# Optimization experiments

Measured on AMD Instinct MI355X. Metric: run time of the kernel, lower is better.

The kernel has to match this reference:

```python
import jax, jax.numpy as jnp
import numpy as np

WS = 8          # window_size
NH = 8          # num_heads
VD = 512        # values_dim
CD = 128        # coords_dim
INNER = 512     # inner_ratio * values_dim
E = INNER // NH # head_dim = 64
B, Hh, Ww_ = 2, 224, 224

# relative position indices (static)
_idx = np.array([[x, y] for x in range(WS) for y in range(WS)])
_rel = _idx[None, :, :] - _idx[:, None, :] + WS - 1  # (WS^2, WS^2, 2)
REL0 = jnp.asarray(_rel[:, :, 0])
REL1 = jnp.asarray(_rel[:, :, 1])

# shifted-window masks (static)
_s = WS * (WS // 2)
_rm = np.zeros((WS * WS, WS * WS), np.float32)
_rm[-_s:, :-_s] = -np.inf
_rm[:-_s, -_s:] = -np.inf
_cm = _rm.reshape(WS, WS, WS, WS).transpose(1, 0, 3, 2).reshape(WS * WS, WS * WS)
ROW_MASK = jnp.asarray(_rm)
COL_MASK = jnp.asarray(_cm)


def _rmsnorm(x, g, eps=1e-6):
    return x * g * jax.lax.rsqrt(jnp.mean(x * x, axis=-1, keepdims=True) + eps)


def _to_windows(x, b, Wh, Ww):
    # x: (b, hp, wp, INNER) with channel layout (e H) (head fastest)
    x = x.reshape(b, Wh, WS, Ww, WS, E, NH)
    return x.transpose(0, 6, 1, 3, 2, 4, 5).reshape(b, NH, Wh, Ww, WS * WS, E)


def setup_inputs() -> dict:
    key = jax.random.key(0)
    ks = jax.random.split(key, 8)
    s = 0.02
    return {
        "embedded_values": jax.random.normal(ks[0], (B, Hh, Ww_, VD), jnp.float32),
        "embedded_coords": jax.random.normal(ks[1], (B, Hh, Ww_, CD), jnp.float32),
        "Wqk_v": jax.random.normal(ks[2], (VD, 2 * INNER), jnp.float32) * s,
        "bqk_v": jnp.zeros((2 * INNER,), jnp.float32),
        "g_v": jnp.ones((2 * INNER,), jnp.float32),
        "Wv": jax.random.normal(ks[3], (VD, INNER), jnp.float32) * s,
        "bv": jnp.zeros((INNER,), jnp.float32),
        "Wqk_c": jax.random.normal(ks[4], (CD, 2 * INNER), jnp.float32) * s,
        "bqk_c": jnp.zeros((2 * INNER,), jnp.float32),
        "g_c": jnp.ones((2 * INNER,), jnp.float32),
        "pos_emb": jax.random.normal(ks[5], (2 * WS - 1, 2 * WS - 1), jnp.float32),
        "Wout": jax.random.normal(ks[6], (INNER, VD), jnp.float32) * s,
        "bout": jnp.zeros((VD,), jnp.float32),
    }


def reference(embedded_values, embedded_coords, Wqk_v, bqk_v, g_v, Wv, bv,
              Wqk_c, bqk_c, g_c, pos_emb, Wout, bout):
    b, h, w, _ = embedded_values.shape
    # projections; torch concat then rearrange '(d k)' k=3 interleaves channels -> reshape (..., INNER, 3)
    vqk = _rmsnorm(embedded_values @ Wqk_v + bqk_v, g_v)          # (b,h,w,2*INNER)
    vval = embedded_values @ Wv + bv                               # (b,h,w,INNER)
    v = jnp.concatenate([vqk, vval], axis=-1).reshape(b, h, w, INNER, 3)
    c = _rmsnorm(embedded_coords @ Wqk_c + bqk_c, g_c).reshape(b, h, w, INNER, 2)

    pad_h = (-h) % WS
    pad_w = (-w) % WS
    v = jnp.pad(v, ((0, 0), (0, pad_h), (0, pad_w), (0, 0), (0, 0)))
    c = jnp.pad(c, ((0, 0), (0, pad_h), (0, pad_w), (0, 0), (0, 0)))
    # shifted=True: roll windows by half window (no inverse roll in original)
    v = jnp.roll(v, (-(WS // 2), -(WS // 2)), axis=(1, 2))
    c = jnp.roll(c, (-(WS // 2), -(WS // 2)), axis=(1, 2))

    hp, wp = h + pad_h, w + pad_w
    Wh, Ww = hp // WS, wp // WS
    qv = _to_windows(v[..., 0], b, Wh, Ww)
    kv = _to_windows(v[..., 1], b, Wh, Ww)
    vv = _to_windows(v[..., 2], b, Wh, Ww)
    qc = _to_windows(c[..., 0], b, Wh, Ww)
    kc = _to_windows(c[..., 1], b, Wh, Ww)

    scale = float(E) ** 0.5
    dots = (jnp.einsum('bhijpe,bhijqe->bhijpq', qv, kv)
            + jnp.einsum('bhijpe,bhijqe->bhijpq', qc, kc)) / scale
    dots = dots + pos_emb[REL0, REL1]
    # shifted-window masks on last window row / column
    dots = dots.at[:, :, -1, :].add(ROW_MASK)
    dots = dots.at[:, :, :, -1].add(COL_MASK)

    attn = jax.nn.softmax(dots, axis=-1)
    y = jnp.einsum('bhijpq,bhijqe->bhijpe', attn, vv)
    # un-window; output channel layout is (H e) (head slow)
    y = y.reshape(b, NH, Wh, Ww, WS, WS, E).transpose(0, 2, 4, 3, 5, 1, 6)
    y = y.reshape(b, hp, wp, INNER)[:, :h, :w, :]
    return y @ Wout + bout
```

## Files before the change

### kernel.cpp

```cpp
#include <hip/hip_runtime.h>


using u16 = unsigned short;
typedef short bf16x8 __attribute__((ext_vector_type(8)));
typedef float f32x4 __attribute__((ext_vector_type(4)));
typedef u16 u16x4 __attribute__((ext_vector_type(4)));
typedef u16 u16x8 __attribute__((ext_vector_type(8)));

__device__ __forceinline__ float bf2f(u16 v) {
  return __uint_as_float(((unsigned)v) << 16);
}
__device__ __forceinline__ u16 f2bf(float f) {
  unsigned u = __float_as_uint(f);
  u += 0x7fffu + ((u >> 16) & 1u);
  return (u16)(u >> 16);
}

__device__ __forceinline__ void gld16(const u16* g, u16* l) {
  __builtin_amdgcn_global_load_lds(
      (const __attribute__((address_space(1))) unsigned*)g,
      (__attribute__((address_space(3))) unsigned*)l, 16, 0, 0);
}

struct f8 { float v[8]; };
__device__ __forceinline__ f8 ld8(const float* p) {
  f8 r;
  *(float4*)&r.v[0] = *(const float4*)p;
  *(float4*)&r.v[4] = *(const float4*)(p + 4);
  return r;
}
__device__ __forceinline__ bf16x8 nfrag(u16x8 raw, const f8& A, const f8& B, float s) {
  u16x8 o;
#pragma unroll
  for (int j = 0; j < 8; ++j) o[j] = f2bf(bf2f(raw[j]) * (A.v[j] * s + B.v[j]));
  return *(bf16x8*)&o;
}
__device__ __forceinline__ bf16x8 nfragA(u16x8 raw, const f8& A, float s) {
  u16x8 o;
#pragma unroll
  for (int j = 0; j < 8; ++j) o[j] = f2bf(bf2f(raw[j]) * (A.v[j] * s));
  return *(bf16x8*)&o;
}

__global__ void conv_bf16(const float* __restrict__ in, u16* __restrict__ out) {
  size_t i = ((size_t)blockIdx.x * 256 + threadIdx.x) * 8;
  float4 a = *(const float4*)(in + i);
  float4 b = *(const float4*)(in + i + 4);
  u16x8 o;
  o[0] = f2bf(a.x); o[1] = f2bf(a.y); o[2] = f2bf(a.z); o[3] = f2bf(a.w);
  o[4] = f2bf(b.x); o[5] = f2bf(b.y); o[6] = f2bf(b.z); o[7] = f2bf(b.w);
  *(u16x8*)(out + i) = o;
}

__global__ void prep_wv(const float* __restrict__ Wqkv, const float* __restrict__ Wv,
                        u16* __restrict__ out) {
  int idx = blockIdx.x * 256 + threadIdx.x;
  if (idx >= 1536 * 512) return;
  int j = idx >> 9, kk = idx & 511;
  int t = j >> 9, rr = j & 511, nn = rr >> 6, e = rr & 63;
  int cc = 3 * (e * 8 + nn) + t;
  float v = (cc < 1024) ? Wqkv[kk * 1024 + cc] : Wv[kk * 512 + (cc - 1024)];
  out[idx] = f2bf(v);
}

__global__ void prep_wc(const float* __restrict__ W, u16* __restrict__ out) {
  int idx = blockIdx.x * 256 + threadIdx.x;
  if (idx >= 1024 * 128) return;
  int j = idx >> 7, kk = idx & 127;
  int t = j >> 9, rr = j & 511, nn = rr >> 6, e = rr & 63;
  int cc = 2 * (e * 8 + nn) + t;
  out[idx] = f2bf(W[kk * 1024 + cc]);
}

__global__ void prep_wout(const float* __restrict__ W, u16* __restrict__ out) {
  int idx = blockIdx.x * 256 + threadIdx.x;
  if (idx >= 512 * 512) return;
  int o = idx >> 9, kk = idx & 511;
  out[idx] = f2bf(W[kk * 512 + o]);
}

__global__ void prep_vec(const float* __restrict__ bqkv, const float* __restrict__ g_v,
                         const float* __restrict__ bv, const float* __restrict__ bqkc,
                         const float* __restrict__ g_c,
                         float* __restrict__ bpv, float* __restrict__ gAv, float* __restrict__ gBv,
                         float* __restrict__ bpc, float* __restrict__ gAc, float* __restrict__ gBc) {
  int j = blockIdx.x * 256 + threadIdx.x;
  if (j < 1536) {
    int t = j >> 9, rr = j & 511, nn = rr >> 6, e = rr & 63;
    int cc = 3 * (e * 8 + nn) + t;
    if (cc < 1024) { bpv[j] = bqkv[cc]; gAv[j] = g_v[cc]; gBv[j] = 0.f; }
    else           { bpv[j] = bv[cc - 1024]; gAv[j] = 0.f; gBv[j] = 1.f; }
  }
  if (j < 1024) {
    int t = j >> 9, rr = j & 511, nn = rr >> 6, e = rr & 63;
    int cc = 2 * (e * 8 + nn) + t;
    bpc[j] = bqkc[cc]; gAc[j] = g_c[cc]; gBc[j] = 0.f;
  }
}

__global__ void prep_biasT(const float* __restrict__ pe, float* __restrict__ bT) {
  int idx = blockIdx.x * 256 + threadIdx.x;
  if (idx >= 4 * 4096) return;
  int v = idx >> 12, q = (idx >> 6) & 63, p = idx & 63;
  int ap = p >> 3, bp = p & 7, aq = q >> 3, bq = q & 7;
  float val = pe[(aq - ap + 7) * 15 + (bq - bp + 7)];
  if ((v & 1) && ((ap >= 4) != (aq >= 4))) val = -1e30f;
  if ((v & 2) && ((bp >= 4) != (bq >= 4))) val = -1e30f;
  bT[idx] = val;
}

template<int N, int K, int MODE>
__global__ __launch_bounds__(256, 4) void gemm_bt(
    const u16* __restrict__ A, const u16* __restrict__ Bt,
    const float* __restrict__ bias, void* __restrict__ outp,
    float* __restrict__ part, const float* __restrict__ gB, int nwg) {
  constexpr int NCB = N / 128;
  constexpr int KT = K / 32;
  const int orig = blockIdx.x;
  const int work = (orig & 7) * (nwg >> 3) + (orig >> 3);
  const int bm = work / NCB, bn = work % NCB;

  const int tid = threadIdx.x;
  const int w = tid >> 6;
  const int lane = tid & 63;
  const int wr = w >> 1, wc = w & 1;
  const int g = lane >> 4, c = lane & 15;

  __shared__ u16 As[2 * 4096];
  __shared__ u16 Bs[2 * 4096];

  f32x4 acc[4][4] = {};
  const u16* Ag = A + (size_t)bm * 128 * K;
  const u16* Bg = Bt + (size_t)bn * 128 * K;

  auto stage = [&](int buf, int kt) {
    const int k0 = kt * 32;
#pragma unroll
    for (int i = 0; i < 2; ++i) {
      const int idx = i * 256 + tid;
      const int row = idx >> 2, ch = idx & 3;
      const int sch = ch ^ ((row >> 1) & 3);
      gld16(Ag + (size_t)row * K + k0 + sch * 8, As + buf * 4096 + idx * 8);
      gld16(Bg + (size_t)row * K + k0 + sch * 8, Bs + buf * 4096 + idx * 8);
    }
  };

  stage(0, 0);
  __syncthreads();

  const int swz = (c >> 1) & 3;
  for (int kt = 0; kt < KT; ++kt) {
    if (kt + 1 < KT) stage((kt + 1) & 1, kt + 1);
    const u16* Ab = As + (kt & 1) * 4096;
    const u16* Bb = Bs + (kt & 1) * 4096;
    bf16x8 af[4], bfv[4];
#pragma unroll
    for (int mi = 0; mi < 4; ++mi)
      af[mi] = *(const bf16x8*)(Ab + (wr * 64 + mi * 16 + c) * 32 + (g ^ swz) * 8);
#pragma unroll
    for (int ni = 0; ni < 4; ++ni)
      bfv[ni] = *(const bf16x8*)(Bb + (wc * 64 + ni * 16 + c) * 32 + (g ^ swz) * 8);
#pragma unroll
    for (int mi = 0; mi < 4; ++mi)
#pragma unroll
      for (int ni = 0; ni < 4; ++ni)
        acc[mi][ni] = __builtin_amdgcn_mfma_f32_16x16x32_bf16(bfv[ni], af[mi], acc[mi][ni], 0, 0, 0);
    __syncthreads();
  }

  const int rowbase = bm * 128 + wr * 64;
  const int colbase = bn * 128 + wc * 64;
  if constexpr (MODE == 0) {
    u16* O = (u16*)outp;
    float rowsq[4] = {0.f, 0.f, 0.f, 0.f};
#pragma unroll
    for (int ni = 0; ni < 4; ++ni) {
      const int col4 = colbase + ni * 16 + g * 4;
      const float4 bb = *(const float4*)(bias + col4);
      const float4 gb = *(const float4*)(gB + col4);
#pragma unroll
      for (int mi = 0; mi < 4; ++mi) {
        const int row = rowbase + mi * 16 + c;
        u16x4 pk;
        float v0 = acc[mi][ni][0] + bb.x;
        float v1 = acc[mi][ni][1] + bb.y;
        float v2 = acc[mi][ni][2] + bb.z;
        float v3 = acc[mi][ni][3] + bb.w;
        pk[0] = f2bf(v0); pk[1] = f2bf(v1); pk[2] = f2bf(v2); pk[3] = f2bf(v3);
        *(u16x4*)(O + (size_t)row * N + col4) = pk;
        rowsq[mi] += (gb.x == 0.f ? v0 * v0 : 0.f) + (gb.y == 0.f ? v1 * v1 : 0.f)
                   + (gb.z == 0.f ? v2 * v2 : 0.f) + (gb.w == 0.f ? v3 * v3 : 0.f);
      }
    }
#pragma unroll
    for (int mi = 0; mi < 4; ++mi) {
      float s = rowsq[mi];
      s += __shfl_xor(s, 16);
      s += __shfl_xor(s, 32);
      rowsq[mi] = s;
    }
    float* red = (float*)As;
    if (g == 0) {
#pragma unroll
      for (int mi = 0; mi < 4; ++mi)
        red[wc * 128 + wr * 64 + mi * 16 + c] = rowsq[mi];
    }
    __syncthreads();
    if (tid < 128)
      part[(size_t)(bm * 128 + tid) * NCB + bn] = red[tid] + red[128 + tid];
  } else {
    float* O = (float*)outp;
#pragma unroll
    for (int ni = 0; ni < 4; ++ni) {
      const int col4 = colbase + ni * 16 + g * 4;
      const float4 bb = *(const float4*)(bias + col4);
#pragma unroll
      for (int mi = 0; mi < 4; ++mi) {
        const int row = rowbase + mi * 16 + c;
        f32x4 o;
        o[0] = acc[mi][ni][0] + bb.x;
        o[1] = acc[mi][ni][1] + bb.y;
        o[2] = acc[mi][ni][2] + bb.z;
        o[3] = acc[mi][ni][3] + bb.w;
        *(f32x4*)(O + (size_t)row * N + col4) = o;
      }
    }
  }
}

__global__ void combine_scales(const float* __restrict__ pvp, const float* __restrict__ pcp,
                               float* __restrict__ sv, float* __restrict__ sc) {
  const int i = blockIdx.x * 256 + threadIdx.x;
  float s = 0.f;
#pragma unroll
  for (int k = 0; k < 12; ++k) s += pvp[(size_t)i * 12 + k];
  sv[i] = rsqrtf(s * (1.f / 1024.f) + 1e-6f);
  float s2 = 0.f;
#pragma unroll
  for (int k = 0; k < 8; ++k) s2 += pcp[(size_t)i * 8 + k];
  sc[i] = rsqrtf(s2 * (1.f / 1024.f) + 1e-6f);
}

__global__ __launch_bounds__(64) void attn_kernel(
    const u16* __restrict__ Pv, const u16* __restrict__ Pc,
    const float* __restrict__ sv, const float* __restrict__ sc,
    const float* __restrict__ gAv, const float* __restrict__ gBv,
    const float* __restrict__ gAc, const float* __restrict__ gBc,
    const float* __restrict__ biasT, u16* __restrict__ Y) {
  const int l = threadIdx.x;
  int bx = blockIdx.x;
  const int wj = bx % 28; bx /= 28;
  const int wi = bx % 28; bx /= 28;
  const int n = bx & 7;
  const int bi = bx >> 3;

  const int g = l >> 4, c = l & 15;
  const int rr0 = l >> 3, rch = l & 7;

  __shared__ u16 Vl[64 * 72];
  __shared__ u16 Pl[64 * 72];

  auto pixof = [&](int a, int b2) -> int {
    int y = wi * 8 + a + 4; if (y >= 224) y -= 224;
    int x = wj * 8 + b2 + 4; if (x >= 224) x -= 224;
    return (bi * 224 + y) * 224 + x;
  };

  int pixr[4]; float svr[4], scr[4];
#pragma unroll
  for (int r = 0; r < 4; ++r) {
    const int p = r * 16 + c;
    pixr[r] = pixof(p >> 3, p & 7);
    svr[r] = sv[pixr[r]];
    scr[r] = sc[pixr[r]];
  }

  u16x8 vreg[8]; float vs_[8];
#pragma unroll
  for (int i = 0; i < 8; ++i) {
    const int pix = pixof(i, rr0);
    vs_[i] = sv[pix];
    vreg[i] = *(const u16x8*)(Pv + (size_t)pix * 1536 + 1024 + n * 64 + rch * 8);
  }

  f32x4 acc[4][4] = {};
#pragma unroll
  for (int kk = 0; kk < 2; ++kk) {
    const int e0 = kk * 32 + g * 8;
    const f8 qA = ld8(gAv + n * 64 + e0), qB = ld8(gBv + n * 64 + e0);
    const f8 kA = ld8(gAv + 512 + n * 64 + e0), kB = ld8(gBv + 512 + n * 64 + e0);
    bf16x8 af[4], bq[4];
#pragma unroll
    for (int r = 0; r < 4; ++r) {
      const u16* src = Pv + (size_t)pixr[r] * 1536 + n * 64 + e0;
      af[r] = nfrag(*(const u16x8*)(src + 512), kA, kB, svr[r]);
      bq[r] = nfrag(*(const u16x8*)src, qA, qB, svr[r]);
    }
#pragma unroll
    for (int mi = 0; mi < 4; ++mi)
#pragma unroll
      for (int ni = 0; ni < 4; ++ni)
        acc[mi][ni] = __builtin_amdgcn_mfma_f32_16x16x32_bf16(af[mi], bq[ni], acc[mi][ni], 0, 0, 0);
  }
#pragma unroll
  for (int kk = 0; kk < 2; ++kk) {
    const int e0 = kk * 32 + g * 8;
    const f8 qA = ld8(gAc + n * 64 + e0);
    const f8 kA = ld8(gAc + 512 + n * 64 + e0);
    bf16x8 af[4], bq[4];
#pragma unroll
    for (int r = 0; r < 4; ++r) {
      const u16* src = Pc + (size_t)pixr[r] * 1024 + n * 64 + e0;
      af[r] = nfragA(*(const u16x8*)(src + 512), kA, scr[r]);
      bq[r] = nfragA(*(const u16x8*)src, qA, scr[r]);
    }
#pragma unroll
    for (int mi = 0; mi < 4; ++mi)
#pragma unroll
      for (int ni = 0; ni < 4; ++ni)
        acc[mi][ni] = __builtin_amdgcn_mfma_f32_16x16x32_bf16(af[mi], bq[ni], acc[mi][ni], 0, 0, 0);
  }

  const int variant = ((wi == 27) ? 1 : 0) | ((wj == 27) ? 2 : 0);
  const float* BT = biasT + variant * 4096;
#pragma unroll
  for (int mi = 0; mi < 4; ++mi)
#pragma unroll
    for (int ni = 0; ni < 4; ++ni)
#pragma unroll
      for (int r = 0; r < 4; ++r) {
        const int q = mi * 16 + g * 4 + r;
        const int p = ni * 16 + c;
        acc[mi][ni][r] = acc[mi][ni][r] * 0.125f + BT[q * 64 + p];
      }
  float rinv[4];
#pragma unroll
  for (int ni = 0; ni < 4; ++ni) {
    float m = -3.0e38f;
#pragma unroll
    for (int mi = 0; mi < 4; ++mi)
#pragma unroll
      for (int r = 0; r < 4; ++r) m = fmaxf(m, acc[mi][ni][r]);
    m = fmaxf(m, __shfl_xor(m, 16));
    m = fmaxf(m, __shfl_xor(m, 32));
    float ssum = 0.f;
#pragma unroll
    for (int mi = 0; mi < 4; ++mi)
#pragma unroll
      for (int r = 0; r < 4; ++r) {
        float e = __expf(acc[mi][ni][r] - m);
        acc[mi][ni][r] = e;
        ssum += e;
      }
    ssum += __shfl_xor(ssum, 16);
    ssum += __shfl_xor(ssum, 32);
    rinv[ni] = 1.f / ssum;
  }

#pragma unroll
  for (int mi = 0; mi < 4; ++mi)
#pragma unroll
    for (int ni = 0; ni < 4; ++ni) {
      u16x4 pk;
#pragma unroll
      for (int r = 0; r < 4; ++r) pk[r] = f2bf(acc[mi][ni][r] * rinv[ni]);
      *(u16x4*)(Pl + (ni * 16 + c) * 72 + mi * 16 + g * 4) = pk;
    }
  {
    const f8 vA = ld8(gAv + 1024 + n * 64 + rch * 8);
    const f8 vB = ld8(gBv + 1024 + n * 64 + rch * 8);
#pragma unroll
    for (int i = 0; i < 8; ++i) {
      bf16x8 nv = nfrag(vreg[i], vA, vB, vs_[i]);
      *(bf16x8*)(Vl + (i * 8 + rr0) * 72 + rch * 8) = nv;
    }
  }

  f32x4 ya[4][4] = {};
#pragma unroll
  for (int kk = 0; kk < 2; ++kk) {
    bf16x8 pa[4];
#pragma unroll
    for (int mi = 0; mi < 4; ++mi)
      pa[mi] = *(const bf16x8*)(Pl + (mi * 16 + c) * 72 + kk * 32 + g * 8);
#pragma unroll
    for (int ni = 0; ni < 4; ++ni) {
      u16x8 vtmp;
#pragma unroll
      for (int j = 0; j < 8; ++j)
        vtmp[j] = Vl[(kk * 32 + g * 8 + j) * 72 + ni * 16 + c];
      bf16x8 vb = *(bf16x8*)&vtmp;
#pragma unroll
      for (int mi = 0; mi < 4; ++mi)
        ya[mi][ni] = __builtin_amdgcn_mfma_f32_16x16x32_bf16(pa[mi], vb, ya[mi][ni], 0, 0, 0);
    }
  }

  u16* Yt = Pl;
#pragma unroll
  for (int mi = 0; mi < 4; ++mi)
#pragma unroll
    for (int ni = 0; ni < 4; ++ni) {
      u16x4 yk;
#pragma unroll
      for (int r = 0; r < 4; ++r) yk[r] = f2bf(ya[mi][ni][r]);
      *(u16x4*)(Yt + (ni * 16 + c) * 72 + mi * 16 + g * 4) = yk;
    }
#pragma unroll
  for (int it = 0; it < 8; ++it) {
    const int b2 = l >> 3;
    const int ch = l & 7;
    const int p = it * 8 + b2;
    u16x8 row;
#pragma unroll
    for (int j = 0; j < 8; ++j) row[j] = Yt[(ch * 8 + j) * 72 + p];
    const int oy = wi * 8 + it, ox = wj * 8 + b2;
    *(u16x8*)(Y + ((size_t)(bi * 224 + oy) * 224 + ox) * 512 + n * 64 + ch * 8) = row;
  }
}

extern "C" void kernel_launch(void* const* d_in, const int* in_sizes, int n_in,
                              void* d_out, int out_size, void* d_ws, size_t ws_size,
                              hipStream_t stream) {
  const float* ev   = (const float*)d_in[0];
  const float* ec   = (const float*)d_in[1];
  const float* Wqkv = (const float*)d_in[2];
  const float* bqkv = (const float*)d_in[3];
  const float* g_v  = (const float*)d_in[4];
  const float* Wv   = (const float*)d_in[5];
  const float* bv   = (const float*)d_in[6];
  const float* Wqkc = (const float*)d_in[7];
  const float* bqkc = (const float*)d_in[8];
  const float* g_c  = (const float*)d_in[9];
  const float* pe   = (const float*)d_in[10];
  const float* Wout = (const float*)d_in[11];
  const float* bout = (const float*)d_in[12];
  float* out = (float*)d_out;

  char* w = (char*)d_ws;
  auto take = [&](size_t b) { char* p = w; w += (b + 255) & ~(size_t)255; return p; };
  u16* Wvp   = (u16*)take(1536ull * 512 * 2);
  u16* Wcp   = (u16*)take(1024ull * 128 * 2);
  u16* Wob   = (u16*)take(512ull * 512 * 2);
  float* bpv = (float*)take(1536 * 4);
  float* gAv = (float*)take(1536 * 4);
  float* gBv = (float*)take(1536 * 4);
  float* bpc = (float*)take(1024 * 4);
  float* gAc = (float*)take(1024 * 4);
  float* gBc = (float*)take(1024 * 4);
  float* bT  = (float*)take(4 * 4096 * 4);
  u16* Pv    = (u16*)take(100352ull * 1536 * 2);
  u16* Pc    = (u16*)take(100352ull * 1024 * 2);
  float* pvp = (float*)take(100352ull * 12 * 4);
  float* pcp = (float*)take(100352ull * 8 * 4);
  float* sv  = (float*)take(100352ull * 4);
  float* sc  = (float*)take(100352ull * 4);
  u16* Yb    = (u16*)take(100352ull * 512 * 2);
  u16* evb   = Yb;
  u16* ecb   = (u16*)take(100352ull * 128 * 2);

  conv_bf16<<<25088, 256, 0, stream>>>(ev, evb);
  conv_bf16<<<6272, 256, 0, stream>>>(ec, ecb);
  prep_wv<<<3072, 256, 0, stream>>>(Wqkv, Wv, Wvp);
  prep_wc<<<512, 256, 0, stream>>>(Wqkc, Wcp);
  prep_wout<<<1024, 256, 0, stream>>>(Wout, Wob);
  prep_vec<<<6, 256, 0, stream>>>(bqkv, g_v, bv, bqkc, g_c, bpv, gAv, gBv, bpc, gAc, gBc);
  prep_biasT<<<64, 256, 0, stream>>>(pe, bT);

  gemm_bt<1536, 512, 0><<<9408, 256, 0, stream>>>(evb, Wvp, bpv, Pv, pvp, gBv, 9408);
  gemm_bt<1024, 128, 0><<<6272, 256, 0, stream>>>(ecb, Wcp, bpc, Pc, pcp, gBc, 6272);
  combine_scales<<<392, 256, 0, stream>>>(pvp, pcp, sv, sc);
  attn_kernel<<<12544, 64, 0, stream>>>(Pv, Pc, sv, sc, gAv, gBv, gAc, gBc, bT, Yb);
  gemm_bt<512, 512, 1><<<3136, 256, 0, stream>>>(Yb, Wob, bout, out, nullptr, nullptr, 3136);
}
```

Measured before the change: 743.5 us.

## Enlarge GEMM tiles to 256x256 with 512 threads and deeper K pipeline

Reworks the bf16 MFMA GEMM from 128x128 tiles with 256 threads to 256x256 tiles with 512 threads and a 64-wide K step. Two stages are kept in flight, with explicit vmcnt and lgkmcnt waits and barriers, and setprio is raised around the MFMA bursts. The aim is more operand reuse per LDS load, less global traffic and better overlap of loads with compute. The per-row square-sum partials shrink to match the new column-block count. In exchange the kernel uses much more LDS (128KB) and registers per block, which lowers occupancy, and for the small-K coords GEMM the pipeline is very short.

```diff
diff --git a/kernel.cpp b/kernel.cpp
--- a/kernel.cpp
+++ b/kernel.cpp
@@ -110,76 +110,111 @@
 }
 
 template<int N, int K, int MODE>
-__global__ __launch_bounds__(256, 4) void gemm_bt(
+__global__ __launch_bounds__(512, 2) void gemm_bt(
     const u16* __restrict__ A, const u16* __restrict__ Bt,
     const float* __restrict__ bias, void* __restrict__ outp,
     float* __restrict__ part, const float* __restrict__ gB, int nwg) {
-  constexpr int NCB = N / 128;
-  constexpr int KT = K / 32;
+  constexpr int NCB = N / 256;
+  constexpr int KT = K / 64;
   const int orig = blockIdx.x;
   const int work = (orig & 7) * (nwg >> 3) + (orig >> 3);
   const int bm = work / NCB, bn = work % NCB;
 
   const int tid = threadIdx.x;
-  const int w = tid >> 6;
+  const int wid = tid >> 6;
   const int lane = tid & 63;
-  const int wr = w >> 1, wc = w & 1;
+  const int wr = wid >> 2, wc = wid & 3;
   const int g = lane >> 4, c = lane & 15;
 
-  __shared__ u16 As[2 * 4096];
-  __shared__ u16 Bs[2 * 4096];
-
-  f32x4 acc[4][4] = {};
-  const u16* Ag = A + (size_t)bm * 128 * K;
-  const u16* Bg = Bt + (size_t)bn * 128 * K;
+  __shared__ u16 As[2 * 2 * 8192];
+  __shared__ u16 Bs[2 * 2 * 8192];
+
+  f32x4 acc[8][4] = {};
+  const u16* Ag = A + (size_t)bm * 256 * K;
+  const u16* Bg = Bt + (size_t)bn * 256 * K;
 
   auto stage = [&](int buf, int kt) {
-    const int k0 = kt * 32;
-#pragma unroll
-    for (int i = 0; i < 2; ++i) {
-      const int idx = i * 256 + tid;
-      const int row = idx >> 2, ch = idx & 3;
-      const int sch = ch ^ ((row >> 1) & 3);
-      gld16(Ag + (size_t)row * K + k0 + sch * 8, As + buf * 4096 + idx * 8);
-      gld16(Bg + (size_t)row * K + k0 + sch * 8, Bs + buf * 4096 + idx * 8);
+    const int k0 = kt * 64;
+#pragma unroll
+    for (int h = 0; h < 2; ++h) {
+#pragma unroll
+      for (int i = 0; i < 2; ++i) {
+        const int idx = i * 512 + tid;
+        const int row = idx >> 3, ch = idx & 7;
+        const int sch = (ch & 4) | ((ch & 3) ^ ((row >> 1) & 3));
+        gld16(Ag + (size_t)(h * 128 + row) * K + k0 + sch * 8,
+              As + (buf * 2 + h) * 8192 + idx * 8);
+        gld16(Bg + (size_t)(h * 128 + row) * K + k0 + sch * 8,
+              Bs + (buf * 2 + h) * 8192 + idx * 8);
+      }
     }
   };
 
   stage(0, 0);
-  __syncthreads();
+  stage(1, 1);
+  asm volatile("s_waitcnt vmcnt(8)" ::: "memory");
+  __builtin_amdgcn_s_barrier();
 
   const int swz = (c >> 1) & 3;
+  const int brow0 = (wc & 1) * 64;
   for (int kt = 0; kt < KT; ++kt) {
-    if (kt + 1 < KT) stage((kt + 1) & 1, kt + 1);
-    const u16* Ab = As + (kt & 1) * 4096;
-    const u16* Bb = Bs + (kt & 1) * 4096;
-    bf16x8 af[4], bfv[4];
-#pragma unroll
-    for (int mi = 0; mi < 4; ++mi)
-      af[mi] = *(const bf16x8*)(Ab + (wr * 64 + mi * 16 + c) * 32 + (g ^ swz) * 8);
+    const int buf = kt & 1;
+    const u16* Ab = As + (buf * 2 + wr) * 8192;
+    const u16* Bb = Bs + (buf * 2 + (wc >> 1)) * 8192;
+
+    bf16x8 a0[8], b0[4];
+#pragma unroll
+    for (int mi = 0; mi < 8; ++mi)
+      a0[mi] = *(const bf16x8*)(Ab + (mi * 16 + c) * 64 + (g ^ swz) * 8);
 #pragma unroll
     for (int ni = 0; ni < 4; ++ni)
-      bfv[ni] = *(const bf16x8*)(Bb + (wc * 64 + ni * 16 + c) * 32 + (g ^ swz) * 8);
-#pragma unroll
-    for (int mi = 0; mi < 4; ++mi)
+      b0[ni] = *(const bf16x8*)(Bb + (brow0 + ni * 16 + c) * 64 + (g ^ swz) * 8);
+    __builtin_amdgcn_s_setprio(1);
+#pragma unroll
+    for (int mi = 0; mi < 8; ++mi)
 #pragma unroll
       for (int ni = 0; ni < 4; ++ni)
-        acc[mi][ni] = __builtin_amdgcn_mfma_f32_16x16x32_bf16(bfv[ni], af[mi], acc[mi][ni], 0, 0, 0);
-    __syncthreads();
-  }
-
-  const int rowbase = bm * 128 + wr * 64;
-  const int colbase = bn * 128 + wc * 64;
+        acc[mi][ni] = __builtin_amdgcn_mfma_f32_16x16x32_bf16(b0[ni], a0[mi], acc[mi][ni], 0, 0, 0);
+    __builtin_amdgcn_s_setprio(0);
+    __builtin_amdgcn_sched_barrier(0);
+
+    bf16x8 a1[8], b1[4];
+#pragma unroll
+    for (int mi = 0; mi < 8; ++mi)
+      a1[mi] = *(const bf16x8*)(Ab + (mi * 16 + c) * 64 + 32 + (g ^ swz) * 8);
+#pragma unroll
+    for (int ni = 0; ni < 4; ++ni)
+      b1[ni] = *(const bf16x8*)(Bb + (brow0 + ni * 16 + c) * 64 + 32 + (g ^ swz) * 8);
+    asm volatile("s_waitcnt lgkmcnt(0)" ::: "memory");
+    __builtin_amdgcn_s_barrier();
+    if (kt + 2 < KT) stage(buf, kt + 2);
+    __builtin_amdgcn_s_setprio(1);
+#pragma unroll
+    for (int mi = 0; mi < 8; ++mi)
+#pragma unroll
+      for (int ni = 0; ni < 4; ++ni)
+        acc[mi][ni] = __builtin_amdgcn_mfma_f32_16x16x32_bf16(b1[ni], a1[mi], acc[mi][ni], 0, 0, 0);
+    __builtin_amdgcn_s_setprio(0);
+    __builtin_amdgcn_sched_barrier(0);
+    if (kt + 2 < KT) asm volatile("s_waitcnt vmcnt(8)" ::: "memory");
+    else             asm volatile("s_waitcnt vmcnt(0)" ::: "memory");
+    __builtin_amdgcn_s_barrier();
+  }
+
+  const int rowbase = bm * 256 + wr * 128;
+  const int colbase = bn * 256 + wc * 64;
   if constexpr (MODE == 0) {
     u16* O = (u16*)outp;
-    float rowsq[4] = {0.f, 0.f, 0.f, 0.f};
+    float rowsq[8];
+#pragma unroll
+    for (int mi = 0; mi < 8; ++mi) rowsq[mi] = 0.f;
 #pragma unroll
     for (int ni = 0; ni < 4; ++ni) {
       const int col4 = colbase + ni * 16 + g * 4;
       const float4 bb = *(const float4*)(bias + col4);
       const float4 gb = *(const float4*)(gB + col4);
 #pragma unroll
-      for (int mi = 0; mi < 4; ++mi) {
+      for (int mi = 0; mi < 8; ++mi) {
         const int row = rowbase + mi * 16 + c;
         u16x4 pk;
         float v0 = acc[mi][ni][0] + bb.x;
@@ -193,21 +228,23 @@
       }
     }
 #pragma unroll
-    for (int mi = 0; mi < 4; ++mi) {
+    for (int mi = 0; mi < 8; ++mi) {
       float s = rowsq[mi];
       s += __shfl_xor(s, 16);
       s += __shfl_xor(s, 32);
       rowsq[mi] = s;
     }
+    __syncthreads();
     float* red = (float*)As;
     if (g == 0) {
 #pragma unroll
-      for (int mi = 0; mi < 4; ++mi)
-        red[wc * 128 + wr * 64 + mi * 16 + c] = rowsq[mi];
+      for (int mi = 0; mi < 8; ++mi)
+        red[wc * 256 + wr * 128 + mi * 16 + c] = rowsq[mi];
     }
     __syncthreads();
-    if (tid < 128)
-      part[(size_t)(bm * 128 + tid) * NCB + bn] = red[tid] + red[128 + tid];
+    if (tid < 256)
+      part[(size_t)(bm * 256 + tid) * NCB + bn] =
+          red[tid] + red[256 + tid] + red[512 + tid] + red[768 + tid];
   } else {
     float* O = (float*)outp;
 #pragma unroll
@@ -215,7 +252,7 @@
       const int col4 = colbase + ni * 16 + g * 4;
       const float4 bb = *(const float4*)(bias + col4);
 #pragma unroll
-      for (int mi = 0; mi < 4; ++mi) {
+      for (int mi = 0; mi < 8; ++mi) {
         const int row = rowbase + mi * 16 + c;
         f32x4 o;
         o[0] = acc[mi][ni][0] + bb.x;
@@ -233,11 +270,11 @@
   const int i = blockIdx.x * 256 + threadIdx.x;
   float s = 0.f;
 #pragma unroll
-  for (int k = 0; k < 12; ++k) s += pvp[(size_t)i * 12 + k];
+  for (int k = 0; k < 6; ++k) s += pvp[(size_t)i * 6 + k];
   sv[i] = rsqrtf(s * (1.f / 1024.f) + 1e-6f);
   float s2 = 0.f;
 #pragma unroll
-  for (int k = 0; k < 8; ++k) s2 += pcp[(size_t)i * 8 + k];
+  for (int k = 0; k < 4; ++k) s2 += pcp[(size_t)i * 4 + k];
   sc[i] = rsqrtf(s2 * (1.f / 1024.f) + 1e-6f);
 }
 
@@ -451,8 +488,8 @@
   float* bT  = (float*)take(4 * 4096 * 4);
   u16* Pv    = (u16*)take(100352ull * 1536 * 2);
   u16* Pc    = (u16*)take(100352ull * 1024 * 2);
-  float* pvp = (float*)take(100352ull * 12 * 4);
-  float* pcp = (float*)take(100352ull * 8 * 4);
+  float* pvp = (float*)take(100352ull * 6 * 4);
+  float* pcp = (float*)take(100352ull * 4 * 4);
   float* sv  = (float*)take(100352ull * 4);
   float* sc  = (float*)take(100352ull * 4);
   u16* Yb    = (u16*)take(100352ull * 512 * 2);
@@ -467,9 +504,9 @@
   prep_vec<<<6, 256, 0, stream>>>(bqkv, g_v, bv, bqkc, g_c, bpv, gAv, gBv, bpc, gAc, gBc);
   prep_biasT<<<64, 256, 0, stream>>>(pe, bT);
 
-  gemm_bt<1536, 512, 0><<<9408, 256, 0, stream>>>(evb, Wvp, bpv, Pv, pvp, gBv, 9408);
-  gemm_bt<1024, 128, 0><<<6272, 256, 0, stream>>>(ecb, Wcp, bpc, Pc, pcp, gBc, 6272);
+  gemm_bt<1536, 512, 0><<<2352, 512, 0, stream>>>(evb, Wvp, bpv, Pv, pvp, gBv, 2352);
+  gemm_bt<1024, 128, 0><<<1568, 512, 0, stream>>>(ecb, Wcp, bpc, Pc, pcp, gBc, 1568);
   combine_scales<<<392, 256, 0, stream>>>(pvp, pcp, sv, sc);
   attn_kernel<<<12544, 64, 0, stream>>>(Pv, Pc, sv, sc, gAv, gBv, gAc, gBc, bT, Yb);
-  gemm_bt<512, 512, 1><<<3136, 256, 0, stream>>>(Yb, Wob, bout, out, nullptr, nullptr, 3136);
-}
+  gemm_bt<512, 512, 1><<<784, 512, 0, stream>>>(Yb, Wob, bout, out, nullptr, nullptr, 784);
+}
```

Result: slower. 780.4 us (+5.0%).
